# Performance work log

Measured on AMD Instinct MI355X. Metric: run time of the kernel, lower is better.

## Reference

```python
import jax, jax.numpy as jnp
import numpy as np

B, S, INPUT_DIM = 8, 512, 64
D_MODEL, NUM_LAYERS, OUTPUT_DIM = 512, 4, 10
D_INNER, D_STATE, D_CONV, DT_RANK = 2 * D_MODEL, 16, 4, 32
GRID_SIZE, SPLINE_K = 5, 3
N_COEFF = GRID_SIZE + SPLINE_K  # 8
_H = 2.0 / GRID_SIZE
GRID = jnp.linspace(-1.0 - SPLINE_K * _H, 1.0 + SPLINE_K * _H, GRID_SIZE + 2 * SPLINE_K + 1)


def b_splines(x):
    # x: (..., in) -> (..., in, N_COEFF) via Cox-de Boor recursion on fixed GRID
    x = x[..., None]
    b = ((x >= GRID[:-1]) & (x < GRID[1:])).astype(x.dtype)
    for p in range(1, SPLINE_K + 1):
        left = (x - GRID[:-(p + 1)]) / (GRID[p:-1] - GRID[:-(p + 1)])
        right = (GRID[p + 1:] - x) / (GRID[p + 1:] - GRID[1:-p])
        b = left * b[..., :-1] + right * b[..., 1:]
    return b


def kan(x, base_w, spline_w):
    # efficient-KAN: silu base path + per-edge spline path
    return jax.nn.silu(x) @ base_w.T + jnp.einsum('...ik,oik->...o', b_splines(x), spline_w)


def layernorm(x, g, b):
    m = jnp.mean(x, -1, keepdims=True)
    v = jnp.var(x, -1, keepdims=True)
    return (x - m) / jnp.sqrt(v + 1e-5) * g + b


def liquid_proj(x, Win, Wrec, b, tau):
    # liquid time-constant RNN: h' = (tanh(Wx + Uh + b) - h) / tau
    pre = x @ Win  # (B,S,H)
    tau_pos = jax.nn.softplus(tau) + 0.1
    def step(h, p):
        act = jnp.tanh(p + h @ Wrec + b)
        h = h + (act - h) / tau_pos
        return h, h
    h0 = jnp.zeros((x.shape[0], Win.shape[1]), x.dtype)
    hT, hs = jax.lax.scan(step, h0, pre.transpose(1, 0, 2))
    return hs.transpose(1, 0, 2), hT


def mamba_block(x, in_proj_w, conv_w, conv_b, x_proj_w, dt_proj_w, dt_proj_b, A_log, Dp, out_proj_w):
    Bb, Ss, _ = x.shape
    xz = x @ in_proj_w.T                       # (B,S,2*di)
    xm, z = jnp.split(xz, 2, axis=-1)
    # causal depthwise conv1d with kernel D_CONV
    xp = jnp.pad(xm, ((0, 0), (D_CONV - 1, 0), (0, 0)))
    xm = sum(xp[:, k:k + Ss, :] * conv_w[:, k] for k in range(D_CONV)) + conv_b
    xm = jax.nn.silu(xm)
    x_dbl = xm @ x_proj_w.T                    # (B,S,dt_rank+2n)
    dt, Bc, Cc = jnp.split(x_dbl, [DT_RANK, DT_RANK + D_STATE], axis=-1)
    dt = jax.nn.softplus(dt @ dt_proj_w.T + dt_proj_b)   # (B,S,di)
    A = -jnp.exp(A_log)                        # (di,n)
    dA = jnp.exp(dt[..., None] * A)            # (B,S,di,n)
    dBu = dt[..., None] * Bc[:, :, None, :] * xm[..., None]
    def step(h, inp):
        a, bu, c = inp
        h = a * h + bu
        return h, jnp.einsum('bdn,bn->bd', h, c)
    h0 = jnp.zeros((Bb, D_INNER, D_STATE), x.dtype)
    _, ys = jax.lax.scan(step, h0, (dA.transpose(1, 0, 2, 3), dBu.transpose(1, 0, 2, 3), Cc.transpose(1, 0, 2)))
    y = ys.transpose(1, 0, 2) + Dp * xm
    y = y * jax.nn.silu(z)
    return y @ out_proj_w.T


def forward(x, lq_Win, lq_Wrec, lq_b, lq_tau, ln_g, ln_b, in_proj_w, conv_w, conv_b,
            x_proj_w, dt_proj_w, dt_proj_b, A_log, Dp, out_proj_w,
            kan_base_w, kan_spline_w, fn_g, fn_b, cls_base_w, cls_spline_w):
    x, _ = liquid_proj(x, lq_Win, lq_Wrec, lq_b, lq_tau)
    for l in range(NUM_LAYERS):
        residual = x
        xn = layernorm(x, ln_g[l], ln_b[l])
        xm = mamba_block(xn, in_proj_w[l], conv_w[l], conv_b[l], x_proj_w[l],
                         dt_proj_w[l], dt_proj_b[l], A_log[l], Dp[l], out_proj_w[l])
        x = residual + kan(xm, kan_base_w[l], kan_spline_w[l])
    x = layernorm(x, fn_g, fn_b)
    return kan(x.mean(axis=1), cls_base_w, cls_spline_w)


def setup_inputs():
    key = jax.random.key(0)
    ks = jax.random.split(key, 12)
    n = lambda k, shape, s: jax.random.normal(k, shape, jnp.float32) * s
    return {
        "x": n(ks[0], (B, S, INPUT_DIM), 1.0),
        "lq_Win": n(ks[1], (INPUT_DIM, D_MODEL), INPUT_DIM ** -0.5),
        "lq_Wrec": n(ks[2], (D_MODEL, D_MODEL), D_MODEL ** -0.5),
        "lq_b": jnp.zeros((D_MODEL,), jnp.float32),
        "lq_tau": jnp.ones((D_MODEL,), jnp.float32),
        "ln_g": jnp.ones((NUM_LAYERS, D_MODEL), jnp.float32),
        "ln_b": jnp.zeros((NUM_LAYERS, D_MODEL), jnp.float32),
        "in_proj_w": n(ks[3], (NUM_LAYERS, 2 * D_INNER, D_MODEL), D_MODEL ** -0.5),
        "conv_w": n(ks[4], (NUM_LAYERS, D_INNER, D_CONV), D_CONV ** -0.5),
        "conv_b": jnp.zeros((NUM_LAYERS, D_INNER), jnp.float32),
        "x_proj_w": n(ks[5], (NUM_LAYERS, DT_RANK + 2 * D_STATE, D_INNER), D_INNER ** -0.5),
        "dt_proj_w": n(ks[6], (NUM_LAYERS, D_INNER, DT_RANK), DT_RANK ** -0.5),
        "dt_proj_b": jnp.full((NUM_LAYERS, D_INNER), float(np.log(np.expm1(0.01))), jnp.float32),
        "A_log": jnp.log(jnp.broadcast_to(jnp.arange(1, D_STATE + 1, dtype=jnp.float32), (NUM_LAYERS, D_INNER, D_STATE))),
        "Dp": jnp.ones((NUM_LAYERS, D_INNER), jnp.float32),
        "out_proj_w": n(ks[7], (NUM_LAYERS, D_MODEL, D_INNER), D_INNER ** -0.5),
        "kan_base_w": n(ks[8], (NUM_LAYERS, D_MODEL, D_MODEL), D_MODEL ** -0.5),
        "kan_spline_w": n(ks[9], (NUM_LAYERS, D_MODEL, D_MODEL, N_COEFF), 0.1 * D_MODEL ** -0.5),
        "fn_g": jnp.ones((D_MODEL,), jnp.float32),
        "fn_b": jnp.zeros((D_MODEL,), jnp.float32),
        "cls_base_w": n(ks[10], (OUTPUT_DIM, D_MODEL), D_MODEL ** -0.5),
        "cls_spline_w": n(ks[11], (OUTPUT_DIM, D_MODEL, N_COEFF), 0.1 * D_MODEL ** -0.5),
    }


def reference(x, lq_Win, lq_Wrec, lq_b, lq_tau, ln_g, ln_b, in_proj_w, conv_w, conv_b,
              x_proj_w, dt_proj_w, dt_proj_b, A_log, Dp, out_proj_w,
              kan_base_w, kan_spline_w, fn_g, fn_b, cls_base_w, cls_spline_w):
    return forward(x, lq_Win, lq_Wrec, lq_b, lq_tau, ln_g, ln_b, in_proj_w, conv_w, conv_b,
                   x_proj_w, dt_proj_w, dt_proj_b, A_log, Dp, out_proj_w,
                   kan_base_w, kan_spline_w, fn_g, fn_b, cls_base_w, cls_spline_w)
```

## Files before the change

### kernel.cpp

```cpp
#include <hip/hip_runtime.h>
#include <hip/hip_bf16.h>
#include <cmath>

#define DEV __device__ __forceinline__

constexpr int B_ = 8, S_ = 512, IN_ = 64, D_ = 512, L_ = 4;
constexpr int DI_ = 1024, DCONV_ = 4, DTR_ = 32;
constexpr int ROWS = B_ * S_;

constexpr size_t MB = 1ull << 20;
constexpr size_t OFF_X    = 0;
constexpr size_t OFF_XN   = OFF_X   + 8*MB;
constexpr size_t OFF_XZ   = OFF_XN  + 8*MB;
constexpr size_t OFF_XM   = OFF_XZ  + 32*MB;
constexpr size_t OFF_DT   = OFF_XM  + 16*MB;
constexpr size_t OFF_XDBL = OFF_DT  + 16*MB;
constexpr size_t OFF_YG   = OFF_XDBL+ 1*MB;
constexpr size_t OFF_MO   = OFF_YG  + 16*MB;
constexpr size_t OFF_WINT = OFF_MO  + 8*MB;
constexpr size_t OFF_MEAN = OFF_WINT+ 128*1024;
constexpr size_t OFF_HBUF = OFF_MEAN+ 16*1024;
constexpr size_t OFF_FLG  = OFF_HBUF+ 32*1024;
constexpr size_t OFF_W16  = OFF_FLG + 64*1024;
constexpr size_t OFF_BASIS= OFF_XZ;

constexpr size_t W_IP = 0;
constexpr size_t W_OP = 1048576;
constexpr size_t W_KB = 1572864;
constexpr size_t W_KS = 1835008;
constexpr size_t W_XP = 3932160;
constexpr size_t W_DT = 3997696;
constexpr size_t W_PER_LAYER = 4030464;

DEV float siluf(float x){ return x / (1.f + __expf(-x)); }
DEV float softplusf(float x){ return fmaxf(x, 0.f) + log1pf(__expf(-fabsf(x))); }
DEV unsigned short f2h(float f){ return __builtin_bit_cast(unsigned short, (_Float16)f); }
DEV float h2f(unsigned short u){ return (float)__builtin_bit_cast(_Float16, u); }
DEV int pk2(float a, float b){ return (int)((unsigned)f2h(a) | ((unsigned)f2h(b) << 16)); }

typedef _Float16 half8 __attribute__((ext_vector_type(8)));
typedef float f32x4 __attribute__((ext_vector_type(4)));

DEV void bspline8(float x, float* bb){
  const float h = 0.4f, g0 = -2.2f;
  float b0[11];
#pragma unroll
  for (int j = 0; j < 11; ++j){
    float gj  = g0 + h * j;
    float gj1 = g0 + h * (j + 1);
    b0[j] = (x >= gj && x < gj1) ? 1.f : 0.f;
  }
#pragma unroll
  for (int p = 1; p <= 3; ++p){
    float inv = 1.f / (h * p);
#pragma unroll
    for (int j = 0; j + p < 11; ++j){
      float gj  = g0 + h * j;
      float gip = g0 + h * (j + p + 1);
      b0[j] = (x - gj) * inv * b0[j] + (gip - x) * inv * b0[j + 1];
    }
  }
#pragma unroll
  for (int c = 0; c < 8; ++c) bb[c] = b0[c];
}

__global__ __launch_bounds__(256)
void conv_w16(const float* __restrict__ ip, const float* __restrict__ op,
              const float* __restrict__ kb, const float* __restrict__ ks,
              const float* __restrict__ xp, unsigned short* __restrict__ w16)
{
  int blk = blockIdx.x, tid = threadIdx.x;
  const float* src; size_t doff; int sb;
  if      (blk < 512) { src = ip; doff = W_IP; sb = blk; }
  else if (blk < 768) { src = op; doff = W_OP; sb = blk - 512; }
  else if (blk < 896) { src = kb; doff = W_KB; sb = blk - 768; }
  else if (blk < 1920){ src = ks; doff = W_KS; sb = blk - 896; }
  else                { src = xp; doff = W_XP; sb = blk - 1920; }
  size_t e = (size_t)sb * 2048 + tid * 8;
  float4 a = *(const float4*)(src + e), b = *(const float4*)(src + e + 4);
  int4 v = { pk2(a.x,a.y), pk2(a.z,a.w), pk2(b.x,b.y), pk2(b.z,b.w) };
  *(int4*)&w16[doff + e] = v;
}

template<bool SILU_A, int EPI>
__global__ __launch_bounds__(256)
void gemm_nt(const float* __restrict__ A, int lda,
             const float* __restrict__ W, int ldw,
             float* __restrict__ C, int ldc,
             const float* __restrict__ bias, int K)
{
  __shared__ float As[16][68];
  __shared__ float Ws[16][68];
  const int tid = threadIdx.x;
  const int m0 = blockIdx.y * 64, n0 = blockIdx.x * 64;
  const int lr = tid >> 2, lc = (tid & 3) * 4;
  const float* Ap = A + (size_t)(m0 + lr) * lda + lc;
  const float* Wp = W + (size_t)(n0 + lr) * ldw + lc;
  const int tx = tid & 15, ty = tid >> 4;
  float acc[4][4] = {};
  for (int k0 = 0; k0 < K; k0 += 16){
    float4 a = *(const float4*)(Ap + k0);
    float4 w = *(const float4*)(Wp + k0);
    if (SILU_A){ a.x = siluf(a.x); a.y = siluf(a.y); a.z = siluf(a.z); a.w = siluf(a.w); }
    __syncthreads();
    As[lc+0][lr] = a.x; As[lc+1][lr] = a.y; As[lc+2][lr] = a.z; As[lc+3][lr] = a.w;
    Ws[lc+0][lr] = w.x; Ws[lc+1][lr] = w.y; Ws[lc+2][lr] = w.z; Ws[lc+3][lr] = w.w;
    __syncthreads();
#pragma unroll
    for (int k = 0; k < 16; ++k){
      float4 av = *(const float4*)&As[k][ty*4];
      float4 wv = *(const float4*)&Ws[k][tx*4];
      acc[0][0] += av.x*wv.x; acc[0][1] += av.x*wv.y; acc[0][2] += av.x*wv.z; acc[0][3] += av.x*wv.w;
      acc[1][0] += av.y*wv.x; acc[1][1] += av.y*wv.y; acc[1][2] += av.y*wv.z; acc[1][3] += av.y*wv.w;
      acc[2][0] += av.z*wv.x; acc[2][1] += av.z*wv.y; acc[2][2] += av.z*wv.z; acc[2][3] += av.z*wv.w;
      acc[3][0] += av.w*wv.x; acc[3][1] += av.w*wv.y; acc[3][2] += av.w*wv.z; acc[3][3] += av.w*wv.w;
    }
  }
#pragma unroll
  for (int i = 0; i < 4; ++i){
    float* Crow = C + (size_t)(m0 + ty*4 + i) * ldc + n0 + tx*4;
    float4 r = {acc[i][0], acc[i][1], acc[i][2], acc[i][3]};
    *(float4*)Crow = r;
  }
}


template<int AMODE>
DEV void stage_a(const void* Av, int lda, int m0, int sr, int k0, int sh,
                 int4& av0, int4& av1)
{
  if (AMODE == 0){
    const unsigned short* ag = (const unsigned short*)Av + (size_t)(m0 + sr) * lda + k0 + sh*16;
    av0 = *(const int4*)ag; av1 = *(const int4*)(ag + 8);
  } else {
    const float* ag = (const float*)Av + (size_t)(m0 + sr) * lda + k0 + sh*16;
    float4 a0 = *(const float4*)ag,     a1 = *(const float4*)(ag+4);
    float4 a2 = *(const float4*)(ag+8), a3 = *(const float4*)(ag+12);
    if (AMODE == 2){
      a0.x=siluf(a0.x); a0.y=siluf(a0.y); a0.z=siluf(a0.z); a0.w=siluf(a0.w);
      a1.x=siluf(a1.x); a1.y=siluf(a1.y); a1.z=siluf(a1.z); a1.w=siluf(a1.w);
      a2.x=siluf(a2.x); a2.y=siluf(a2.y); a2.z=siluf(a2.z); a2.w=siluf(a2.w);
      a3.x=siluf(a3.x); a3.y=siluf(a3.y); a3.z=siluf(a3.z); a3.w=siluf(a3.w);
    }
    av0 = (int4){ pk2(a0.x,a0.y), pk2(a0.z,a0.w), pk2(a1.x,a1.y), pk2(a1.z,a1.w) };
    av1 = (int4){ pk2(a2.x,a2.y), pk2(a2.z,a2.w), pk2(a3.x,a3.y), pk2(a3.z,a3.w) };
  }
}

DEV void epi_store(int EPI, void* Cv, size_t off, float v)
{
  if (EPI == 0)      ((float*)Cv)[off] = v;
  else if (EPI == 1) ((float*)Cv)[off] += v;
  else if (EPI == 3) ((unsigned short*)Cv)[off] = f2h(v);
  else               atomicAdd((float*)Cv + off, v);
}

template<int AMODE, int EPI>
__global__ __launch_bounds__(256)
void gemm_h128(const void* __restrict__ Av, int lda,
               const unsigned short* __restrict__ W,
               void* __restrict__ Cv, int ldc, int K)
{
  __shared__ unsigned short As[128*40];
  __shared__ unsigned short Bs[128*40];
  const int tid = threadIdx.x;
  const int m0 = blockIdx.y * 128, n0 = blockIdx.x * 128;
  const int wid = tid >> 6, lane = tid & 63;
  const int wm = (wid & 1) * 64, wn = (wid >> 1) * 64;
  const int fr = lane & 15, fk = lane >> 4;
  const int sr = tid >> 1, sh = tid & 1;

  f32x4 acc[4][4];
#pragma unroll
  for (int i = 0; i < 4; ++i)
#pragma unroll
    for (int j = 0; j < 4; ++j)
#pragma unroll
      for (int r = 0; r < 4; ++r) acc[i][j][r] = 0.f;

  for (int k0 = 0; k0 < K; k0 += 32){
    int4 av0, av1;
    stage_a<AMODE>(Av, lda, m0, sr, k0, sh, av0, av1);
    const unsigned short* wg = W + (size_t)(n0 + sr) * K + k0 + sh*16;
    int4 bv0 = *(const int4*)wg, bv1 = *(const int4*)(wg + 8);
    __syncthreads();
    *(int4*)&As[sr*40 + sh*16]     = av0;
    *(int4*)&As[sr*40 + sh*16 + 8] = av1;
    *(int4*)&Bs[sr*40 + sh*16]     = bv0;
    *(int4*)&Bs[sr*40 + sh*16 + 8] = bv1;
    __syncthreads();
    half8 a[4], b[4];
#pragma unroll
    for (int i = 0; i < 4; ++i) a[i] = *(const half8*)&As[(wm + i*16 + fr)*40 + fk*8];
#pragma unroll
    for (int j = 0; j < 4; ++j) b[j] = *(const half8*)&Bs[(wn + j*16 + fr)*40 + fk*8];
#pragma unroll
    for (int i = 0; i < 4; ++i)
#pragma unroll
      for (int j = 0; j < 4; ++j)
        acc[i][j] = __builtin_amdgcn_mfma_f32_16x16x32_f16(a[i], b[j], acc[i][j], 0, 0, 0);
  }
#pragma unroll
  for (int i = 0; i < 4; ++i)
#pragma unroll
    for (int j = 0; j < 4; ++j){
      int col = n0 + wn + j*16 + fr;
#pragma unroll
      for (int r = 0; r < 4; ++r){
        int row = m0 + wm + i*16 + fk*4 + r;
        epi_store(EPI, Cv, (size_t)row * ldc + col, acc[i][j][r]);
      }
    }
}

template<int AMODE, int EPI, int KSPLIT = 1>
__global__ __launch_bounds__(256)
void gemm_h64(const void* __restrict__ Av, int lda,
              const unsigned short* __restrict__ W,
              void* __restrict__ Cv, int ldc, int K)
{
  __shared__ unsigned short As[128*40];
  __shared__ unsigned short Bs[64*40];
  const int tid = threadIdx.x;
  const int m0 = blockIdx.y * 128, n0 = blockIdx.x * 64;
  const int klen = K / KSPLIT, kbase = blockIdx.z * klen;
  const int wid = tid >> 6, lane = tid & 63;
  const int fr = lane & 15, fk = lane >> 4;
  const int sr = tid >> 1, sh = tid & 1;
  const int br = tid >> 2, bq = tid & 3;

  f32x4 acc[2][4];
#pragma unroll
  for (int i = 0; i < 2; ++i)
#pragma unroll
    for (int j = 0; j < 4; ++j)
#pragma unroll
      for (int r = 0; r < 4; ++r) acc[i][j][r] = 0.f;

  for (int kk = 0; kk < klen; kk += 32){
    int k0 = kbase + kk;
    int4 av0, av1;
    stage_a<AMODE>(Av, lda, m0, sr, k0, sh, av0, av1);
    const unsigned short* wg = W + (size_t)(n0 + br) * K + k0 + bq*8;
    int4 bv0 = *(const int4*)wg;
    __syncthreads();
    *(int4*)&As[sr*40 + sh*16]     = av0;
    *(int4*)&As[sr*40 + sh*16 + 8] = av1;
    *(int4*)&Bs[br*40 + bq*8]      = bv0;
    __syncthreads();
    half8 a[2], b[4];
#pragma unroll
    for (int i = 0; i < 2; ++i) a[i] = *(const half8*)&As[(wid*32 + i*16 + fr)*40 + fk*8];
#pragma unroll
    for (int j = 0; j < 4; ++j) b[j] = *(const half8*)&Bs[(j*16 + fr)*40 + fk*8];
#pragma unroll
    for (int i = 0; i < 2; ++i)
#pragma unroll
      for (int j = 0; j < 4; ++j)
        acc[i][j] = __builtin_amdgcn_mfma_f32_16x16x32_f16(a[i], b[j], acc[i][j], 0, 0, 0);
  }
#pragma unroll
  for (int i = 0; i < 2; ++i)
#pragma unroll
    for (int j = 0; j < 4; ++j){
      int col = n0 + j*16 + fr;
#pragma unroll
      for (int r = 0; r < 4; ++r){
        int row = m0 + wid*32 + i*16 + fk*4 + r;
        epi_store(EPI, Cv, (size_t)row * ldc + col, acc[i][j][r]);
      }
    }
}

__global__ __launch_bounds__(256)
void transpose_win(const float* __restrict__ Win, float* __restrict__ WinT)
{
  int idx = blockIdx.x * 256 + threadIdx.x;
  int n = idx >> 6, k = idx & 63;
  WinT[idx] = Win[(size_t)k * 512 + n];
}

__global__ __launch_bounds__(512)
void liquid_scan3(const float* __restrict__ pre, const float* __restrict__ Wrec,
                  const float* __restrict__ bias, const float* __restrict__ tau,
                  float* __restrict__ xout, float* __restrict__ hbuf,
                  unsigned* __restrict__ flags)
{
  __shared__ float Wl[32800];
  __shared__ float hl[544];
  __shared__ float hnew[64];
  const int tid = threadIdx.x;
  const int bid = blockIdx.x;
  const int slice = bid >> 3, b = bid & 7;
  for (int idx = tid; idx < 512*16; idx += 512){
    int k = idx >> 4, c4 = (idx & 15) * 4;
    float4 w = *(const float4*)(Wrec + (size_t)k*512 + slice*64 + c4);
    *(float4*)&Wl[k*64 + c4 + (k>>6)*4] = w;
  }
  hl[tid + (tid>>6)*4] = 0.f;
  const int o = tid >> 3, kl = tid & 7;
  const int og = slice*64 + o;
  const float tauinv = 1.f / (softplusf(tau[og]) + 0.1f);
  const float bo = bias[og];
  float hold = 0.f;
  const float* preb = pre + (size_t)b * S_ * 512;
  float* xb = xout + (size_t)b * S_ * 512;
  float* hb0 = hbuf + (size_t)b * 512;
  unsigned* bflags = flags + b*8*16;
  unsigned* myflag = bflags + slice*16;
  const int kbase = kl * 64;
  const float* wp = &Wl[(size_t)kbase*64 + o + kl*4];
  __syncthreads();
  for (int t = 0; t < S_; ++t){
    float prev = (kl == 0) ? preb[(size_t)t*512 + og] : 0.f;
    float hreg[64];
#pragma unroll
    for (int j4 = 0; j4 < 16; ++j4)
      *(float4*)&hreg[j4*4] = *(const float4*)&hl[kbase + kl*4 + j4*4];
    float s = 0.f;
#pragma unroll
    for (int j = 0; j < 64; ++j)
      s += hreg[j] * wp[(size_t)j * 64];
    s += __shfl_xor(s, 1);
    s += __shfl_xor(s, 2);
    s += __shfl_xor(s, 4);
    if (kl == 0){
      float act = tanhf(s + prev + bo);
      hold += (act - hold) * tauinv;
      xb[(size_t)t*512 + og] = hold;
      hnew[o] = hold;
    }
    __syncthreads();
    if (tid < 64)
      __hip_atomic_store(hb0 + (t&1)*4096 + slice*64 + tid, hnew[tid],
                         __ATOMIC_RELAXED, __HIP_MEMORY_SCOPE_AGENT);
    if (tid == 0){
      asm volatile("s_waitcnt vmcnt(0)" ::: "memory");
      __hip_atomic_store(myflag, (unsigned)(t+1),
                         __ATOMIC_RELAXED, __HIP_MEMORY_SCOPE_AGENT);
    }
    if (tid < 8){
      while (__hip_atomic_load(bflags + tid*16, __ATOMIC_RELAXED,
                               __HIP_MEMORY_SCOPE_AGENT) < (unsigned)(t+1)) { }
    }
    __syncthreads();
    float hv = __hip_atomic_load(hb0 + (t&1)*4096 + tid,
                                 __ATOMIC_RELAXED, __HIP_MEMORY_SCOPE_AGENT);
    hl[tid + (tid>>6)*4] = hv;
    __syncthreads();
  }
}

__global__ __launch_bounds__(256)
void conv_silu(const unsigned short* __restrict__ xz, const float* __restrict__ cw,
               const float* __restrict__ cb, unsigned short* __restrict__ xm)
{
  int idx = blockIdx.x * 256 + threadIdx.x;
  int d = idx & 1023;
  int bs = idx >> 10;
  int t = bs & 511;
  const unsigned short* p = xz + (size_t)bs * 2048 + d;
  float4 w = *(const float4*)(cw + d*4);
  float acc = cb[d] + w.w * h2f(p[0]);
  if (t >= 1) acc += w.z * h2f(p[-2048]);
  if (t >= 2) acc += w.y * h2f(p[-2*2048]);
  if (t >= 3) acc += w.x * h2f(p[-3*2048]);
  xm[idx] = f2h(siluf(acc));
}

__global__ __launch_bounds__(256)
void mamba_scan3(const float* __restrict__ xdbl, const unsigned short* __restrict__ xm,
                 const unsigned short* __restrict__ xz,
                 const float* __restrict__ dt_w, const float* __restrict__ dt_b,
                 const float* __restrict__ A_log, const float* __restrict__ Dp,
                 unsigned short* __restrict__ yg)
{
  const int tid = threadIdx.x;
  const int wave = tid >> 6, lane = tid & 63;
  const int ch = lane >> 3, sub = lane & 7;
  const int d = blockIdx.x * 32 + wave * 8 + ch;
  const int b = blockIdx.y;
  float2 al = *(const float2*)(A_log + (size_t)d*16 + sub*2);
  const float A0 = -__expf(al.x), A1 = -__expf(al.y);
  const float Dv = Dp[d];
  const float4 wq = *(const float4*)(dt_w + (size_t)d*32 + sub*4);
  const float dtbv = dt_b[d];
  float h0 = 0.f, h1 = 0.f;
  const size_t rb = (size_t)b * S_;
  const float* xdp = xdbl + rb*64;
  const unsigned short* xmp = xm + rb*1024 + d;
  const unsigned short* zp  = xz + rb*2048 + 1024 + d;
  float* dummy;
  unsigned short* yp = yg + rb*1024 + d;
#pragma unroll 2
  for (int t = 0; t < S_; ++t){
    const float* xr = xdp + (size_t)t*64;
    float4 xq = *(const float4*)(xr + sub*4);
    float s = xq.x*wq.x + xq.y*wq.y + xq.z*wq.z + xq.w*wq.w;
    s += __shfl_xor(s, 1);
    s += __shfl_xor(s, 2);
    s += __shfl_xor(s, 4);
    float dtv = softplusf(s + dtbv);
    float xv  = h2f(xmp[(size_t)t*1024]);
    float2 B2 = *(const float2*)(xr + 32 + sub*2);
    float2 C2 = *(const float2*)(xr + 48 + sub*2);
    float cbu = dtv * xv;
    h0 = __expf(dtv * A0) * h0 + cbu * B2.x;
    h1 = __expf(dtv * A1) * h1 + cbu * B2.y;
    float y = h0 * C2.x + h1 * C2.y;
    y += __shfl_xor(y, 1);
    y += __shfl_xor(y, 2);
    y += __shfl_xor(y, 4);
    if (sub == 0){
      float zv = h2f(zp[(size_t)t*2048]);
      yp[(size_t)t*1024] = f2h((y + Dv * xv) * siluf(zv));
    }
  }
}

template<bool H>
__global__ __launch_bounds__(256)
void layernorm_k(const float* __restrict__ x, const float* __restrict__ g,
                 const float* __restrict__ b, void* __restrict__ y)
{
  __shared__ float red[8];
  const int row = blockIdx.x, tid = threadIdx.x;
  const float* xr = x + (size_t)row * 512;
  float2 v = *(const float2*)(xr + tid*2);
  float s = v.x + v.y;
#pragma unroll
  for (int o = 32; o; o >>= 1) s += __shfl_xor(s, o);
  if ((tid & 63) == 0) red[tid >> 6] = s;
  __syncthreads();
  float mean = (red[0] + red[1] + red[2] + red[3]) * (1.f/512.f);
  float dx = v.x - mean, dy = v.y - mean;
  float q = dx*dx + dy*dy;
#pragma unroll
  for (int o = 32; o; o >>= 1) q += __shfl_xor(q, o);
  if ((tid & 63) == 0) red[4 + (tid >> 6)] = q;
  __syncthreads();
  float var = (red[4] + red[5] + red[6] + red[7]) * (1.f/512.f);
  float rstd = rsqrtf(var + 1e-5f);
  float2 gg = *(const float2*)(g + tid*2);
  float2 bb = *(const float2*)(b + tid*2);
  float ox = dx*rstd*gg.x + bb.x;
  float oy = dy*rstd*gg.y + bb.y;
  if (H){
    unsigned* yr = (unsigned*)y + (size_t)row*256 + tid;
    *yr = (unsigned)f2h(ox) | ((unsigned)f2h(oy) << 16);
  } else {
    float2 o2 = {ox, oy};
    *(float2*)((float*)y + (size_t)row*512 + tid*2) = o2;
  }
}

__global__ __launch_bounds__(256)
void bspline_kernel(const float* __restrict__ xin, unsigned short* __restrict__ basis)
{
  int idx = blockIdx.x * 256 + threadIdx.x;
  float x = xin[idx];
  float bb[8];
  bspline8(x, bb);
  int4 v = { pk2(bb[0],bb[1]), pk2(bb[2],bb[3]), pk2(bb[4],bb[5]), pk2(bb[6],bb[7]) };
  *(int4*)(basis + (size_t)idx * 8) = v;
}

__global__ __launch_bounds__(512)
void mean_over_s(const float* __restrict__ x, float* __restrict__ out)
{
  int b = blockIdx.x, d = threadIdx.x;
  const float* p = x + (size_t)b*S_*512 + d;
  float s = 0.f;
  for (int t = 0; t < S_; ++t) s += p[(size_t)t*512];
  out[b*512 + d] = s * (1.f/512.f);
}

__global__ __launch_bounds__(64)
void cls_kan(const float* __restrict__ xmean, const float* __restrict__ bw,
             const float* __restrict__ sw, float* __restrict__ out)
{
  int o = blockIdx.x % 10, b = blockIdx.x / 10;
  int lane = threadIdx.x;
  float acc = 0.f;
  for (int i = lane; i < 512; i += 64){
    float xv = xmean[b*512 + i];
    acc += siluf(xv) * bw[o*512 + i];
    float bb[8]; bspline8(xv, bb);
    const float* sp = sw + ((size_t)(o*512 + i)) * 8;
#pragma unroll
    for (int c = 0; c < 8; ++c) acc += bb[c] * sp[c];
  }
#pragma unroll
  for (int off = 32; off; off >>= 1) acc += __shfl_xor(acc, off);
  if (lane == 0) out[b*10 + o] = acc;
}

extern "C" void kernel_launch(void* const* d_in, const int* in_sizes, int n_in,
                              void* d_out, int out_size, void* d_ws, size_t ws_size,
                              hipStream_t stream)
{
  const float* x_in    = (const float*)d_in[0];
  const float* lq_Win  = (const float*)d_in[1];
  const float* lq_Wrec = (const float*)d_in[2];
  const float* lq_b    = (const float*)d_in[3];
  const float* lq_tau  = (const float*)d_in[4];
  const float* ln_g    = (const float*)d_in[5];
  const float* ln_bi   = (const float*)d_in[6];
  const float* in_proj = (const float*)d_in[7];
  const float* conv_w  = (const float*)d_in[8];
  const float* conv_b  = (const float*)d_in[9];
  const float* x_proj  = (const float*)d_in[10];
  const float* dt_w    = (const float*)d_in[11];
  const float* dt_b    = (const float*)d_in[12];
  const float* A_log   = (const float*)d_in[13];
  const float* Dp      = (const float*)d_in[14];
  const float* out_w   = (const float*)d_in[15];
  const float* kb_w    = (const float*)d_in[16];
  const float* ks_w    = (const float*)d_in[17];
  const float* fn_g    = (const float*)d_in[18];
  const float* fn_b    = (const float*)d_in[19];
  const float* cb_w    = (const float*)d_in[20];
  const float* cs_w    = (const float*)d_in[21];
  float* out = (float*)d_out;

  char* ws = (char*)d_ws;
  float* xcur  = (float*)(ws + OFF_X);
  float* xn32  = (float*)(ws + OFF_XN);
  unsigned short* xn16 = (unsigned short*)(ws + OFF_XN);
  unsigned short* xz16 = (unsigned short*)(ws + OFF_XZ);
  unsigned short* xm16 = (unsigned short*)(ws + OFF_XM);
  float* xdbl  = (float*)(ws + OFF_XDBL);
  unsigned short* yg16 = (unsigned short*)(ws + OFF_YG);
  float* mo    = (float*)(ws + OFF_MO);
  float* wint  = (float*)(ws + OFF_WINT);
  float* xmean = (float*)(ws + OFF_MEAN);
  float* hbufp = (float*)(ws + OFF_HBUF);
  unsigned* flgp = (unsigned*)(ws + OFF_FLG);
  unsigned short* w16 = (unsigned short*)(ws + OFF_W16);
  unsigned short* basis = (unsigned short*)(ws + OFF_BASIS);

  transpose_win<<<128, 256, 0, stream>>>(lq_Win, wint);
  gemm_nt<false,0><<<dim3(D_/64, ROWS/64), 256, 0, stream>>>(x_in, IN_, wint, IN_, xn32, D_, nullptr, IN_);
  hipMemsetAsync(flgp, 0, 8*8*16*sizeof(unsigned), stream);
  liquid_scan3<<<64, 512, 0, stream>>>(xn32, lq_Wrec, lq_b, lq_tau, xcur, hbufp, flgp);

  for (int l = 0; l < L_; ++l){
    conv_w16<<<1952, 256, 0, stream>>>(
        in_proj + (size_t)l*2*DI_*D_, out_w + (size_t)l*D_*DI_,
        kb_w + (size_t)l*D_*D_, ks_w + (size_t)l*D_*D_*8,
        x_proj + (size_t)l*64*DI_, w16 + (size_t)l*W_PER_LAYER);
  }

  for (int l = 0; l < L_; ++l){
    const unsigned short* wl = w16 + (size_t)l*W_PER_LAYER;
    layernorm_k<true><<<ROWS, 256, 0, stream>>>(xcur, ln_g + l*D_, ln_bi + l*D_, xn16);
    gemm_h128<0,3><<<dim3(16, 32), 256, 0, stream>>>(
        xn16, D_, wl + W_IP, xz16, 2*DI_, D_);
    conv_silu<<<ROWS*DI_/256, 256, 0, stream>>>(xz16, conv_w + l*DI_*DCONV_, conv_b + l*DI_, xm16);
    hipMemsetAsync(xdbl, 0, (size_t)ROWS*64*sizeof(float), stream);
    gemm_h64<0,5,4><<<dim3(1, 32, 4), 256, 0, stream>>>(
        xm16, DI_, wl + W_XP, xdbl, 64, DI_);
    mamba_scan3<<<dim3(32, 8), 256, 0, stream>>>(
        xdbl, xm16, xz16, dt_w + (size_t)l*DI_*DTR_, dt_b + l*DI_,
        A_log + (size_t)l*DI_*16, Dp + l*DI_, yg16);
    gemm_h64<0,0><<<dim3(8, 32), 256, 0, stream>>>(
        yg16, DI_, wl + W_OP, mo, D_, DI_);
    bspline_kernel<<<ROWS*D_/256, 256, 0, stream>>>(mo, basis);
    gemm_h64<2,1><<<dim3(8, 32), 256, 0, stream>>>(
        mo, D_, wl + W_KB, xcur, D_, D_);
    gemm_h64<0,1><<<dim3(8, 32), 256, 0, stream>>>(
        basis, D_*8, wl + W_KS, xcur, D_, D_*8);
  }

  layernorm_k<false><<<ROWS, 256, 0, stream>>>(xcur, fn_g, fn_b, xn32);
  mean_over_s<<<B_, 512, 0, stream>>>(xn32, xmean);
  cls_kan<<<B_*10, 64, 0, stream>>>(xmean, cb_w, cs_w, out);
}
```

Before: 4.243 ms.

## Move dt projection out of Mamba scan into separate MFMA GEMM with softplus epilogue

The per-timestep dt projection (32-wide dot plus shuffle reduction plus softplus) is taken out of the serial Mamba scan loop. It is now computed by a new fp16 MFMA GEMM over the x_dbl rows, with a bias+softplus epilogue that writes a full fp32 dt buffer. The x_proj GEMM also drops its 4-way K-split with atomics and memset in favour of a single plain-store pass. This shortens the latency-bound scan's critical path, at the cost of an extra kernel launch and 16MB of dt traffic per layer.

```diff
diff --git a/kernel.cpp b/kernel.cpp
--- a/kernel.cpp
+++ b/kernel.cpp
@@ -67,7 +67,8 @@
 __global__ __launch_bounds__(256)
 void conv_w16(const float* __restrict__ ip, const float* __restrict__ op,
               const float* __restrict__ kb, const float* __restrict__ ks,
-              const float* __restrict__ xp, unsigned short* __restrict__ w16)
+              const float* __restrict__ xp, const float* __restrict__ dt,
+              unsigned short* __restrict__ w16)
 {
   int blk = blockIdx.x, tid = threadIdx.x;
   const float* src; size_t doff; int sb;
@@ -75,7 +76,8 @@
   else if (blk < 768) { src = op; doff = W_OP; sb = blk - 512; }
   else if (blk < 896) { src = kb; doff = W_KB; sb = blk - 768; }
   else if (blk < 1920){ src = ks; doff = W_KS; sb = blk - 896; }
-  else                { src = xp; doff = W_XP; sb = blk - 1920; }
+  else if (blk < 1952){ src = xp; doff = W_XP; sb = blk - 1920; }
+  else                { src = dt; doff = W_DT; sb = blk - 1952; }
   size_t e = (size_t)sb * 2048 + tid * 8;
   float4 a = *(const float4*)(src + e), b = *(const float4*)(src + e + 4);
   int4 v = { pk2(a.x,a.y), pk2(a.z,a.w), pk2(b.x,b.y), pk2(b.z,b.w) };
@@ -147,19 +149,21 @@
   }
 }
 
-DEV void epi_store(int EPI, void* Cv, size_t off, float v)
+template<int EPI>
+DEV void epi_store(void* Cv, size_t off, float v, const float* bias, int col)
 {
   if (EPI == 0)      ((float*)Cv)[off] = v;
   else if (EPI == 1) ((float*)Cv)[off] += v;
-  else if (EPI == 3) ((unsigned short*)Cv)[off] = f2h(v);
-  else               atomicAdd((float*)Cv + off, v);
+  else if (EPI == 2) ((float*)Cv)[off] = softplusf(v + bias[col]);
+  else               ((unsigned short*)Cv)[off] = f2h(v);
 }
 
 template<int AMODE, int EPI>
 __global__ __launch_bounds__(256)
 void gemm_h128(const void* __restrict__ Av, int lda,
                const unsigned short* __restrict__ W,
-               void* __restrict__ Cv, int ldc, int K)
+               void* __restrict__ Cv, int ldc,
+               const float* __restrict__ bias, int K)
 {
   __shared__ unsigned short As[128*40];
   __shared__ unsigned short Bs[128*40];
@@ -208,22 +212,22 @@
 #pragma unroll
       for (int r = 0; r < 4; ++r){
         int row = m0 + wm + i*16 + fk*4 + r;
-        epi_store(EPI, Cv, (size_t)row * ldc + col, acc[i][j][r]);
+        epi_store<EPI>(Cv, (size_t)row * ldc + col, acc[i][j][r], bias, col);
       }
     }
 }
 
-template<int AMODE, int EPI, int KSPLIT = 1>
+template<int AMODE, int EPI>
 __global__ __launch_bounds__(256)
 void gemm_h64(const void* __restrict__ Av, int lda,
               const unsigned short* __restrict__ W,
-              void* __restrict__ Cv, int ldc, int K)
+              void* __restrict__ Cv, int ldc,
+              const float* __restrict__ bias, int K)
 {
   __shared__ unsigned short As[128*40];
   __shared__ unsigned short Bs[64*40];
   const int tid = threadIdx.x;
   const int m0 = blockIdx.y * 128, n0 = blockIdx.x * 64;
-  const int klen = K / KSPLIT, kbase = blockIdx.z * klen;
   const int wid = tid >> 6, lane = tid & 63;
   const int fr = lane & 15, fk = lane >> 4;
   const int sr = tid >> 1, sh = tid & 1;
@@ -237,8 +241,7 @@
 #pragma unroll
       for (int r = 0; r < 4; ++r) acc[i][j][r] = 0.f;
 
-  for (int kk = 0; kk < klen; kk += 32){
-    int k0 = kbase + kk;
+  for (int k0 = 0; k0 < K; k0 += 32){
     int4 av0, av1;
     stage_a<AMODE>(Av, lda, m0, sr, k0, sh, av0, av1);
     const unsigned short* wg = W + (size_t)(n0 + br) * K + k0 + bq*8;
@@ -267,7 +270,7 @@
 #pragma unroll
       for (int r = 0; r < 4; ++r){
         int row = m0 + wid*32 + i*16 + fk*4 + r;
-        epi_store(EPI, Cv, (size_t)row * ldc + col, acc[i][j][r]);
+        epi_store<EPI>(Cv, (size_t)row * ldc + col, acc[i][j][r], bias, col);
       }
     }
 }
@@ -369,9 +372,8 @@
 }
 
 __global__ __launch_bounds__(256)
-void mamba_scan3(const float* __restrict__ xdbl, const unsigned short* __restrict__ xm,
-                 const unsigned short* __restrict__ xz,
-                 const float* __restrict__ dt_w, const float* __restrict__ dt_b,
+void mamba_scan2(const float* __restrict__ dt, const unsigned short* __restrict__ xm,
+                 const float* __restrict__ xdbl, const unsigned short* __restrict__ xz,
                  const float* __restrict__ A_log, const float* __restrict__ Dp,
                  unsigned short* __restrict__ yg)
 {
@@ -383,27 +385,20 @@
   float2 al = *(const float2*)(A_log + (size_t)d*16 + sub*2);
   const float A0 = -__expf(al.x), A1 = -__expf(al.y);
   const float Dv = Dp[d];
-  const float4 wq = *(const float4*)(dt_w + (size_t)d*32 + sub*4);
-  const float dtbv = dt_b[d];
   float h0 = 0.f, h1 = 0.f;
   const size_t rb = (size_t)b * S_;
-  const float* xdp = xdbl + rb*64;
+  const float* dtp = dt + rb*1024 + d;
   const unsigned short* xmp = xm + rb*1024 + d;
   const unsigned short* zp  = xz + rb*2048 + 1024 + d;
-  float* dummy;
+  const float* bcp = xdbl + rb*64 + 32 + sub*2;
+  const float* ccp = xdbl + rb*64 + 48 + sub*2;
   unsigned short* yp = yg + rb*1024 + d;
 #pragma unroll 2
   for (int t = 0; t < S_; ++t){
-    const float* xr = xdp + (size_t)t*64;
-    float4 xq = *(const float4*)(xr + sub*4);
-    float s = xq.x*wq.x + xq.y*wq.y + xq.z*wq.z + xq.w*wq.w;
-    s += __shfl_xor(s, 1);
-    s += __shfl_xor(s, 2);
-    s += __shfl_xor(s, 4);
-    float dtv = softplusf(s + dtbv);
+    float dtv = dtp[(size_t)t*1024];
     float xv  = h2f(xmp[(size_t)t*1024]);
-    float2 B2 = *(const float2*)(xr + 32 + sub*2);
-    float2 C2 = *(const float2*)(xr + 48 + sub*2);
+    float2 B2 = *(const float2*)(bcp + (size_t)t*64);
+    float2 C2 = *(const float2*)(ccp + (size_t)t*64);
     float cbu = dtv * xv;
     h0 = __expf(dtv * A0) * h0 + cbu * B2.x;
     h1 = __expf(dtv * A1) * h1 + cbu * B2.y;
@@ -529,6 +524,7 @@
   unsigned short* xn16 = (unsigned short*)(ws + OFF_XN);
   unsigned short* xz16 = (unsigned short*)(ws + OFF_XZ);
   unsigned short* xm16 = (unsigned short*)(ws + OFF_XM);
+  float* dtb   = (float*)(ws + OFF_DT);
   float* xdbl  = (float*)(ws + OFF_XDBL);
   unsigned short* yg16 = (unsigned short*)(ws + OFF_YG);
   float* mo    = (float*)(ws + OFF_MO);
@@ -545,31 +541,32 @@
   liquid_scan3<<<64, 512, 0, stream>>>(xn32, lq_Wrec, lq_b, lq_tau, xcur, hbufp, flgp);
 
   for (int l = 0; l < L_; ++l){
-    conv_w16<<<1952, 256, 0, stream>>>(
+    conv_w16<<<1968, 256, 0, stream>>>(
         in_proj + (size_t)l*2*DI_*D_, out_w + (size_t)l*D_*DI_,
         kb_w + (size_t)l*D_*D_, ks_w + (size_t)l*D_*D_*8,
-        x_proj + (size_t)l*64*DI_, w16 + (size_t)l*W_PER_LAYER);
+        x_proj + (size_t)l*64*DI_, dt_w + (size_t)l*DI_*DTR_,
+        w16 + (size_t)l*W_PER_LAYER);
   }
 
   for (int l = 0; l < L_; ++l){
     const unsigned short* wl = w16 + (size_t)l*W_PER_LAYER;
     layernorm_k<true><<<ROWS, 256, 0, stream>>>(xcur, ln_g + l*D_, ln_bi + l*D_, xn16);
     gemm_h128<0,3><<<dim3(16, 32), 256, 0, stream>>>(
-        xn16, D_, wl + W_IP, xz16, 2*DI_, D_);
+        xn16, D_, wl + W_IP, xz16, 2*DI_, nullptr, D_);
     conv_silu<<<ROWS*DI_/256, 256, 0, stream>>>(xz16, conv_w + l*DI_*DCONV_, conv_b + l*DI_, xm16);
-    hipMemsetAsync(xdbl, 0, (size_t)ROWS*64*sizeof(float), stream);
-    gemm_h64<0,5,4><<<dim3(1, 32, 4), 256, 0, stream>>>(
-        xm16, DI_, wl + W_XP, xdbl, 64, DI_);
-    mamba_scan3<<<dim3(32, 8), 256, 0, stream>>>(
-        xdbl, xm16, xz16, dt_w + (size_t)l*DI_*DTR_, dt_b + l*DI_,
-        A_log + (size_t)l*DI_*16, Dp + l*DI_, yg16);
+    gemm_h64<0,0><<<dim3(1, 32), 256, 0, stream>>>(
+        xm16, DI_, wl + W_XP, xdbl, 64, nullptr, DI_);
+    gemm_h64<1,2><<<dim3(16, 32), 256, 0, stream>>>(
+        xdbl, 64, wl + W_DT, dtb, DI_, dt_b + l*DI_, DTR_);
+    mamba_scan2<<<dim3(32, 8), 256, 0, stream>>>(
+        dtb, xm16, xdbl, xz16, A_log + (size_t)l*DI_*16, Dp + l*DI_, yg16);
     gemm_h64<0,0><<<dim3(8, 32), 256, 0, stream>>>(
-        yg16, DI_, wl + W_OP, mo, D_, DI_);
+        yg16, DI_, wl + W_OP, mo, D_, nullptr, DI_);
     bspline_kernel<<<ROWS*D_/256, 256, 0, stream>>>(mo, basis);
     gemm_h64<2,1><<<dim3(8, 32), 256, 0, stream>>>(
-        mo, D_, wl + W_KB, xcur, D_, D_);
+        mo, D_, wl + W_KB, xcur, D_, nullptr, D_);
     gemm_h64<0,1><<<dim3(8, 32), 256, 0, stream>>>(
-        basis, D_*8, wl + W_KS, xcur, D_, D_*8);
+        basis, D_*8, wl + W_KS, xcur, D_, nullptr, D_*8);
   }
 
   layernorm_k<false><<<ROWS, 256, 0, stream>>>(xcur, fn_g, fn_b, xn32);
```

Result: faster. 3.789 ms (-10.7%).
